# Kernel optimization log

Hardware: AMD Instinct MI355X
Metric: run time of the kernel (lower is better)

Reference implementation:

```python
import jax, jax.numpy as jnp
import numpy as np

B, N, IN_DIM, OUT = 4, 4096, 3, 40
NPTS = [1024, 256, 64, 16]   # base_points // sampling_ratio
K, FIRST_K = 8, 16
EPS = 1e-5

def gelu(t):
    return jax.nn.gelu(t, approximate=False)  # torch nn.GELU default (erf)

def pdist2(a, b):
    # a: (b,d,m), b: (b,d,n) -> squared pairwise distances (b,m,n)
    aa = jnp.sum(a * a, axis=1)[:, :, None]
    bb = jnp.sum(b * b, axis=1)[:, None, :]
    return aa + bb - 2.0 * jnp.einsum('bdm,bdn->bmn', a, b)

def knn_idx(a, b, k):
    # indices of k nearest points of b for each point of a
    return jax.lax.top_k(-pdist2(a, b), k)[1]

def gather_nbr(x, ind):
    # x: (b,d,n), ind: (b,m,k) -> (b,d,m,k)
    b, d, n = x.shape
    m, k = ind.shape[1], ind.shape[2]
    idx = jnp.broadcast_to(ind.reshape(b, 1, m * k), (b, d, m * k))
    return jnp.take_along_axis(x, idx, axis=2).reshape(b, d, m, k)

def bn(x):
    # BatchNorm (training-mode batch stats, gamma=1, beta=0 as at init)
    ax = (0,) + tuple(range(2, x.ndim))
    mu = jnp.mean(x, axis=ax, keepdims=True)
    var = jnp.mean((x - mu) ** 2, axis=ax, keepdims=True)
    return (x - mu) / jnp.sqrt(var + EPS)

def route(x, nbr):
    # (b,d,n),(b,n,k) -> (b,2d,n,k) : cat([neighbor - center, center])
    sel = gather_nbr(x, nbr)
    xc = x[:, :, :, None]
    return jnp.concatenate([sel - xc, jnp.broadcast_to(xc, sel.shape)], axis=1)

def edge_conv(x, l1, l2, sc, k, nbr=None):
    if nbr is None:
        nbr = knn_idx(x, x, k)  # dynamic graph in feature space
    h = jnp.max(jnp.einsum('of,bfnk->bonk', l1, route(x, nbr)), axis=-1)
    h = gelu(bn(h))
    h = jnp.max(jnp.einsum('of,bfnk->bonk', l2, route(h, nbr)), axis=-1)
    short = x if sc is None else jnp.einsum('of,bfn->bon', sc, x)
    return gelu(bn(short + h))

def fps(xyz, m):
    # farthest point sampling; xyz: (b,3,n) -> indices (b,m); start index 0
    pts = jnp.transpose(xyz, (0, 2, 1))  # (b,n,3)
    b, n, _ = pts.shape
    def body(carry, _):
        dmin, last = carry
        lp = jnp.take_along_axis(pts, last[:, None, None], axis=1)  # (b,1,3)
        d = jnp.sum((pts - lp) ** 2, axis=-1)
        dmin = jnp.minimum(dmin, d)
        nxt = jnp.argmax(dmin, axis=-1).astype(jnp.int32)
        return (dmin, nxt), last
    init = (jnp.full((b, n), jnp.inf, pts.dtype), jnp.zeros((b,), jnp.int32))
    _, inds = jax.lax.scan(body, init, None, length=m)
    return jnp.transpose(inds)  # (b,m)

def _forward(x, xyz, mlp_w, mlp_b, c0_l1, c0_l2, l1s, l2s, scs,
             head_w1, head_w2, head_b2):
    b = x.shape[0]
    nbr0 = knn_idx(xyz, xyz, FIRST_K)
    h = gelu(bn(jnp.einsum('oi,bin->bon', mlp_w, x) + mlp_b[None, :, None]))
    h = edge_conv(h, c0_l1, c0_l2, None, FIRST_K, nbr=nbr0)
    cur = xyz
    for i in range(4):
        m = NPTS[i]
        sind = fps(cur, m)
        sxyz = jnp.take_along_axis(
            cur, jnp.broadcast_to(sind[:, None, :], (b, cur.shape[1], m)), axis=2)
        nbr = knn_idx(sxyz, cur, K)
        cur = jnp.mean(gather_nbr(cur, nbr), axis=-1)      # sampled xyz = nbr mean
        h = jnp.max(gather_nbr(h, nbr), axis=-1)           # sampled feat = nbr max
        h = edge_conv(h, l1s[i], l2s[i], scs[i], K)
    g = jnp.mean(h, axis=-1)                               # global average pool
    g = gelu(bn(g @ head_w1.T))
    return g @ head_w2.T + head_b2[None, :]


def setup_inputs() -> dict:
    key = jax.random.key(0)
    ks = jax.random.split(key, 20)
    def w(k, o, i):
        return (jax.random.normal(k, (o, i), jnp.float32) / np.sqrt(i)).astype(jnp.float32)
    return {
        'x': jax.random.normal(ks[0], (B, IN_DIM, N), jnp.float32),
        'xyz': jax.random.normal(ks[1], (B, 3, N), jnp.float32),
        'mlp_w': w(ks[2], 64, IN_DIM), 'mlp_b': jnp.zeros((64,), jnp.float32),
        'c0_l1': w(ks[3], 64, 128), 'c0_l2': w(ks[4], 64, 128),
        's0_l1': w(ks[5], 64, 128), 's0_l2': w(ks[6], 64, 128),
        's1_l1': w(ks[7], 128, 128), 's1_l2': w(ks[8], 128, 256), 's1_sc': w(ks[9], 128, 64),
        's2_l1': w(ks[10], 256, 256), 's2_l2': w(ks[11], 256, 512), 's2_sc': w(ks[12], 256, 128),
        's3_l1': w(ks[13], 512, 512), 's3_l2': w(ks[14], 512, 1024), 's3_sc': w(ks[15], 512, 256),
        'head_w1': w(ks[16], 256, 512), 'head_w2': w(ks[17], OUT, 256),
        'head_b2': jnp.zeros((OUT,), jnp.float32),
    }


def reference(x, xyz, mlp_w, mlp_b, c0_l1, c0_l2, s0_l1, s0_l2,
              s1_l1, s1_l2, s1_sc, s2_l1, s2_l2, s2_sc, s3_l1, s3_l2, s3_sc,
              head_w1, head_w2, head_b2):
    return _forward(x, xyz, mlp_w, mlp_b, c0_l1, c0_l2,
                    (s0_l1, s1_l1, s2_l1, s3_l1),
                    (s0_l2, s1_l2, s2_l2, s3_l2),
                    (None, s1_sc, s2_sc, s3_sc),
                    head_w1, head_w2, head_b2)
```

## Files before the change

### kernel.cpp

```cpp
#include <hip/hip_runtime.h>
#include <math.h>

#define NCHUNK 32
typedef unsigned long long ull;

__device__ __forceinline__ float gelu_f(float v){
  return 0.5f*v*(1.0f+erff(v*0.70710678118654752440f));
}

__device__ __forceinline__ unsigned flipf(float d){
  unsigned u = __float_as_uint(d);
  return (u & 0x80000000u) ? ~u : (u | 0x80000000u);
}

template<int CTRL>
__device__ __forceinline__ ull dpp64(ull k){
  int lo = __builtin_amdgcn_update_dpp(0, (int)(unsigned)k,       CTRL, 0xF, 0xF, true);
  int hi = __builtin_amdgcn_update_dpp(0, (int)(unsigned)(k>>32), CTRL, 0xF, 0xF, true);
  return ((ull)(unsigned)hi<<32) | (unsigned)lo;
}
__device__ __forceinline__ ull rl64(ull k, int l){
  unsigned lo = (unsigned)__builtin_amdgcn_readlane((int)(unsigned)k, l);
  unsigned hi = (unsigned)__builtin_amdgcn_readlane((int)(unsigned)(k>>32), l);
  return ((ull)hi<<32) | lo;
}
__device__ __forceinline__ ull fmax64(ull a, ull b){
  return (ull)__double_as_longlong(fmax(__longlong_as_double((long long)a),
                                        __longlong_as_double((long long)b)));
}
__device__ __forceinline__ ull wave_fmax(ull k){
  k = fmax64(k, dpp64<0xB1>(k));
  k = fmax64(k, dpp64<0x4E>(k));
  k = fmax64(k, dpp64<0x141>(k));
  k = fmax64(k, dpp64<0x140>(k));
  ull a=rl64(k,0), b=rl64(k,16), c=rl64(k,32), d=rl64(k,48);
  return fmax64(fmax64(a,b), fmax64(c,d));
}
template<int CTRL>
__device__ __forceinline__ ull kmin_dpp(ull k){
  ull o = dpp64<CTRL>(k);
  return o < k ? o : k;
}
__device__ __forceinline__ ull wave_kmin(ull k){
  k = kmin_dpp<0xB1>(k);
  k = kmin_dpp<0x4E>(k);
  k = kmin_dpp<0x141>(k);
  k = kmin_dpp<0x140>(k);
  ull a=rl64(k,0), b=rl64(k,16), c=rl64(k,32), d=rl64(k,48);
  ull ab = a < b ? a : b, cd = c < d ? c : d;
  return ab < cd ? ab : cd;
}


template<int K, int T>
__device__ __forceinline__ void knn_body(
    const float* __restrict__ cand, int n,
    const float* __restrict__ qsrc, const int* __restrict__ qidx, int m,
    int* __restrict__ nbr, float* __restrict__ outc,
    int b, int qblk, char* smem)
{
  float* cx = (float*)smem; float* cy = cx+1024; float* cz = cy+1024; float* cbb = cz+1024;
  constexpr int NWV = T/64;
  int wv = threadIdx.x >> 6, lane = threadIdx.x & 63;
  int q = qblk*NWV + wv;
  const float* cb = cand + (size_t)b*3*n;
  int qi = qidx ? qidx[(size_t)b*m + q] : q;
  const float* qb = qsrc + (size_t)b*3*n;
  float qx = qb[qi], qy = qb[n+qi], qz = qb[2*n+qi];
  float aa = (qx*qx + qy*qy) + qz*qz;

  ull a[K];
  #pragma unroll
  for (int k=0;k<K;k++) a[k] = ~0ull;
  ull worst = ~0ull; int wslot = 0;

  for (int base=0; base<n; base+=1024){
    int cnt = min(1024, n-base);
    for (int j=threadIdx.x; j<cnt; j+=T){
      float x=cb[base+j], y=cb[n+base+j], z=cb[2*n+base+j];
      cx[j]=x; cy[j]=y; cz[j]=z; cbb[j]=(x*x+y*y)+z*z;
    }
    __syncthreads();
    int steps = cnt >> 6;
    for (int i=0;i<steps;i++){
      int j = lane + (i<<6);
      float d = aa + cbb[j] - 2.0f*((qx*cx[j]+qy*cy[j])+qz*cz[j]);
      ull key = ((ull)flipf(d)<<32) | (unsigned)(base+j);
      if (key < worst){
        #pragma unroll
        for (int k=0;k<K;k++) if (k==wslot) a[k] = key;
        worst = a[0]; wslot = 0;
        #pragma unroll
        for (int k=1;k<K;k++){
          bool g = a[k] > worst;
          worst = g ? a[k] : worst;
          wslot = g ? k : wslot;
        }
      }
    }
    __syncthreads();
  }

  #pragma unroll
  for (int kk=2; kk<=K; kk<<=1)
    #pragma unroll
    for (int jj=kk>>1; jj>0; jj>>=1)
      #pragma unroll
      for (int i=0;i<K;i++){
        int l = i ^ jj;
        if (l > i){
          bool dirUp = ((i & kk) == 0);
          ull x = a[i], y = a[l];
          bool sw = dirUp ? (x > y) : (x < y);
          a[i] = sw ? y : x;
          a[l] = sw ? x : y;
        }
      }

  ull head = a[0];
  int res[K];
  #pragma unroll
  for (int r=0; r<K; r++){
    ull mk = wave_kmin(head);
    res[r] = (int)(unsigned)mk;
    if (head == mk){
      #pragma unroll
      for (int i2=0;i2<K-1;i2++) a[i2]=a[i2+1];
      a[K-1] = ~0ull;
      head = a[0];
    }
  }
  if (lane == 0){
    int* o = nbr + ((size_t)b*m + q)*K;
    #pragma unroll
    for (int r=0;r<K;r++) o[r] = res[r];
  }
  if (outc != nullptr && lane < 3){
    const float* cd = cb + (size_t)lane*n;
    float s=0;
    #pragma unroll
    for (int k=0;k<K;k++) s += cd[res[k]];
    outc[((size_t)b*3 + lane)*m + q] = s * (1.0f/K);
  }
}

template<int NP, int T, int M>
__device__ __forceinline__ void fps_mw_seg(const float* __restrict__ cur, int n,
                                           int* __restrict__ sind, float* __restrict__ gdmin,
                                           int b, int M0, int M1, char* smem)
{
  constexpr int NW = T/64;
  int tid = threadIdx.x;
  int wv = tid>>6;
  const float* cb = cur + (size_t)b*3*n;
  float4* lp = (float4*)smem;
  ull* wred = (ull*)(smem + sizeof(float4)*NP*T);
  float* gd = gdmin + (size_t)b*n;
  float px[NP], py[NP], pz[NP], dmin[NP];
  unsigned nj[NP];
  #pragma unroll
  for (int s=0;s<NP;s++){
    int j = tid + s*T;
    px[s]=cb[j]; py[s]=cb[n+j]; pz[s]=cb[2*n+j];
    dmin[s] = (M0==0) ? 1e30f : gd[j];
    nj[s] = (unsigned)(~j);
    lp[j] = make_float4(px[s],py[s],pz[s],0.f);
  }
  __syncthreads();
  int ci = (M0==0) ? 0 : sind[(size_t)b*M + (M0-1)];
  float4 w0 = lp[ci];
  float X = w0.x, Y = w0.y, Z = w0.z;
  if (M0==0 && tid==0) sind[(size_t)b*M] = 0;
  __builtin_amdgcn_s_setprio(3);
  int p = 0;
  int s0 = (M0==0) ? 1 : M0;
  for (int step=s0; step<M1; step++){
    ull key[NP];
    #pragma unroll
    for (int s=0;s<NP;s++){
      float dx=px[s]-X, dy=py[s]-Y, dz=pz[s]-Z;
      float d = (dx*dx + dy*dy) + dz*dz;
      float nd = fminf(dmin[s], d);
      dmin[s] = nd;
      key[s] = ((ull)__float_as_uint(nd)<<32) | nj[s];
    }
    #pragma unroll
    for (int w=NP; w>1; w>>=1)
      #pragma unroll
      for (int i=0;i<NP;i++) if (i < (w>>1))
        key[i] = fmax64(key[i], key[i+(w>>1)]);
    ull wk = wave_fmax(key[0]);
    if ((tid&63)==0) wred[p*NW + wv] = wk;
    __syncthreads();
    ull gk = wred[p*NW];
    #pragma unroll
    for (int w=1;w<NW;w++) gk = fmax64(gk, wred[p*NW + w]);
    int gi = (int)(~(unsigned)gk);
    if (tid==0) sind[(size_t)b*M + step] = gi;
    float4 wp = lp[gi];
    X=wp.x; Y=wp.y; Z=wp.z;
    p ^= 1;
  }
  __builtin_amdgcn_s_setprio(0);
  #pragma unroll
  for (int s=0;s<NP;s++) gd[tid + s*T] = dmin[s];
}

template<int NP, int M>
__device__ __forceinline__ void fps_sw_body(const float* __restrict__ cur, int n,
                                            int* __restrict__ sind, int b, char* smem)
{
  int lane = threadIdx.x;
  const float* cb = cur + (size_t)b*3*n;
  float4* lp = (float4*)smem;
  float px[NP], py[NP], pz[NP], dmin[NP];
  unsigned nj[NP];
  #pragma unroll
  for (int s=0;s<NP;s++){
    int j = lane + s*64;
    px[s]=cb[j]; py[s]=cb[n+j]; pz[s]=cb[2*n+j]; dmin[s]=1e30f;
    nj[s] = (unsigned)(~j);
    lp[j] = make_float4(px[s],py[s],pz[s],0.f);
  }
  float X = lp[0].x, Y = lp[0].y, Z = lp[0].z;
  if (lane==0) sind[(size_t)b*M] = 0;
  __builtin_amdgcn_s_setprio(3);
  for (int step=1; step<M; step++){
    ull key[NP];
    #pragma unroll
    for (int s=0;s<NP;s++){
      float dx=px[s]-X, dy=py[s]-Y, dz=pz[s]-Z;
      float d = (dx*dx + dy*dy) + dz*dz;
      float nd = fminf(dmin[s], d);
      dmin[s] = nd;
      key[s] = ((ull)__float_as_uint(nd)<<32) | nj[s];
    }
    #pragma unroll
    for (int w=NP; w>1; w>>=1)
      #pragma unroll
      for (int i=0;i<NP;i++) if (i < (w>>1))
        key[i] = fmax64(key[i], key[i+(w>>1)]);
    ull gk = wave_fmax(key[0]);
    int gi = (int)(~(unsigned)gk);
    if (lane==0) sind[(size_t)b*M + step] = gi;
    float4 wp = lp[gi];
    X=wp.x; Y=wp.y; Z=wp.z;
  }
  __builtin_amdgcn_s_setprio(0);
}

template<bool DUAL, bool BN>
__device__ __forceinline__ void gemm_body(
    const float* __restrict__ A, const float* __restrict__ B,
    float* __restrict__ out0, float* __restrict__ out1,
    int M, int N, int Kd, int lda, int ldb, int ldo, int boff,
    long sA, long sB, long sO, const float* __restrict__ part, float invR,
    int bxi, int byi, int bzi, char* smem)
{
  A += (size_t)bzi * sA; B += (size_t)bzi * sB;
  float* o0 = out0 + (size_t)bzi * sO;
  float* o1 = DUAL ? (out1 + (size_t)bzi * sO) : nullptr;
  int rowBase = byi*64, colBase = bxi*64;
  float (*As)[64]  = (float(*)[64])smem;
  float (*Bs0)[64] = (float(*)[64])(smem + 4096);
  float (*Bs1)[64] = (float(*)[64])(smem + 8192);
  float* mu_s = (float*)(smem + 12288);
  float* var_s = mu_s + 512;
  int tid = threadIdx.x;
  if (BN){
    for (int oo=tid; oo<Kd; oo+=blockDim.x){
      float s=0, q=0;
      #pragma unroll 4
      for (int c=0;c<NCHUNK;c++){
        s += part[(size_t)c*1024 + oo];
        q += part[(size_t)(NCHUNK+c)*1024 + oo];
      }
      float mu = s*invR;
      mu_s[oo] = mu;
      var_s[oo] = q*invR - mu*mu;
    }
    __syncthreads();
  }
  int ty = tid>>4, tx = tid&15;
  float acc0[4][4] = {}, acc1[4][4] = {};
  int lr = tid>>2, lk = (tid&3)*4;
  for (int k0=0; k0<Kd; k0+=16) {
    float4 va = make_float4(0,0,0,0);
    int r = rowBase + lr;
    if (r < M) va = *(const float4*)(A + (size_t)r*lda + k0 + lk);
    if (BN){
      int c = k0 + lk;
      va.x = gelu_f((va.x - mu_s[c+0]) / sqrtf(var_s[c+0] + 1e-5f));
      va.y = gelu_f((va.y - mu_s[c+1]) / sqrtf(var_s[c+1] + 1e-5f));
      va.z = gelu_f((va.z - mu_s[c+2]) / sqrtf(var_s[c+2] + 1e-5f));
      va.w = gelu_f((va.w - mu_s[c+3]) / sqrtf(var_s[c+3] + 1e-5f));
    }
    As[lk+0][lr]=va.x; As[lk+1][lr]=va.y; As[lk+2][lr]=va.z; As[lk+3][lr]=va.w;
    float4 vb = make_float4(0,0,0,0), vb2 = make_float4(0,0,0,0);
    int c2 = colBase + lr;
    if (c2 < N) {
      vb = *(const float4*)(B + (size_t)c2*ldb + k0 + lk);
      if (DUAL) vb2 = *(const float4*)(B + (size_t)c2*ldb + boff + k0 + lk);
    }
    Bs0[lk+0][lr]=vb.x; Bs0[lk+1][lr]=vb.y; Bs0[lk+2][lr]=vb.z; Bs0[lk+3][lr]=vb.w;
    if (DUAL) {
      Bs1[lk+0][lr]=vb2.x-vb.x; Bs1[lk+1][lr]=vb2.y-vb.y;
      Bs1[lk+2][lr]=vb2.z-vb.z; Bs1[lk+3][lr]=vb2.w-vb.w;
    }
    __syncthreads();
    #pragma unroll
    for (int kk=0;kk<16;kk++){
      float4 a  = *(const float4*)&As[kk][ty*4];
      float4 b0 = *(const float4*)&Bs0[kk][tx*4];
      float av[4]={a.x,a.y,a.z,a.w};
      float b0v[4]={b0.x,b0.y,b0.z,b0.w};
      #pragma unroll
      for (int i=0;i<4;i++)
        #pragma unroll
        for (int j=0;j<4;j++) acc0[i][j] = fmaf(av[i], b0v[j], acc0[i][j]);
      if (DUAL) {
        float4 b1 = *(const float4*)&Bs1[kk][tx*4];
        float b1v[4]={b1.x,b1.y,b1.z,b1.w};
        #pragma unroll
        for (int i=0;i<4;i++)
          #pragma unroll
          for (int j=0;j<4;j++) acc1[i][j] = fmaf(av[i], b1v[j], acc1[i][j]);
      }
    }
    __syncthreads();
  }
  #pragma unroll
  for (int i=0;i<4;i++){
    int r = rowBase + ty*4 + i;
    if (r < M) {
      #pragma unroll
      for (int j=0;j<4;j++){
        int c = colBase + tx*4 + j;
        if (c < N) {
          o0[(size_t)r*ldo + c] = acc0[i][j];
          if (DUAL) o1[(size_t)r*ldo + c] = acc1[i][j];
        }
      }
    }
  }
}

template<bool DUAL, bool BN>
__device__ __forceinline__ void gemm_body_g(
    const float* __restrict__ A, const float* __restrict__ B,
    float* __restrict__ out0, float* __restrict__ out1,
    int M, int N, int Kd, int lda, int ldb, int ldo, int boff,
    const float* __restrict__ part, float invR,
    int bxi, int byi, char* smem)
{
  int rowBase = byi*64, colBase = bxi*64;
  float (*As)[64]  = (float(*)[64])smem;
  float (*Bs0)[64] = (float(*)[64])(smem + 4096);
  float (*Bs1)[64] = (float(*)[64])(smem + 8192);
  float* mu_s = (float*)(smem + 12288);
  float* var_s = mu_s + 512;
  int tid = threadIdx.x;
  bool act = tid < 256;
  if (BN){
    for (int oo=tid; oo<Kd; oo+=blockDim.x){
      float s=0, q=0;
      #pragma unroll 4
      for (int c=0;c<NCHUNK;c++){
        s += part[(size_t)c*1024 + oo];
        q += part[(size_t)(NCHUNK+c)*1024 + oo];
      }
      float mu = s*invR;
      mu_s[oo] = mu;
      var_s[oo] = q*invR - mu*mu;
    }
    __syncthreads();
  }
  int ty = tid>>4, tx = tid&15;
  float acc0[4][4] = {}, acc1[4][4] = {};
  int lr = tid>>2, lk = (tid&3)*4;
  for (int k0=0; k0<Kd; k0+=16) {
    if (act){
      float4 va = make_float4(0,0,0,0);
      int r = rowBase + lr;
      if (r < M) va = *(const float4*)(A + (size_t)r*lda + k0 + lk);
      if (BN){
        int c = k0 + lk;
        va.x = gelu_f((va.x - mu_s[c+0]) / sqrtf(var_s[c+0] + 1e-5f));
        va.y = gelu_f((va.y - mu_s[c+1]) / sqrtf(var_s[c+1] + 1e-5f));
        va.z = gelu_f((va.z - mu_s[c+2]) / sqrtf(var_s[c+2] + 1e-5f));
        va.w = gelu_f((va.w - mu_s[c+3]) / sqrtf(var_s[c+3] + 1e-5f));
      }
      As[lk+0][lr]=va.x; As[lk+1][lr]=va.y; As[lk+2][lr]=va.z; As[lk+3][lr]=va.w;
      float4 vb = make_float4(0,0,0,0), vb2 = make_float4(0,0,0,0);
      int c2 = colBase + lr;
      if (c2 < N) {
        vb = *(const float4*)(B + (size_t)c2*ldb + k0 + lk);
        if (DUAL) vb2 = *(const float4*)(B + (size_t)c2*ldb + boff + k0 + lk);
      }
      Bs0[lk+0][lr]=vb.x; Bs0[lk+1][lr]=vb.y; Bs0[lk+2][lr]=vb.z; Bs0[lk+3][lr]=vb.w;
      if (DUAL) {
        Bs1[lk+0][lr]=vb2.x-vb.x; Bs1[lk+1][lr]=vb2.y-vb.y;
        Bs1[lk+2][lr]=vb2.z-vb.z; Bs1[lk+3][lr]=vb2.w-vb.w;
      }
    }
    __syncthreads();
    if (act){
      #pragma unroll
      for (int kk=0;kk<16;kk++){
        float4 a  = *(const float4*)&As[kk][ty*4];
        float4 b0 = *(const float4*)&Bs0[kk][tx*4];
        float av[4]={a.x,a.y,a.z,a.w};
        float b0v[4]={b0.x,b0.y,b0.z,b0.w};
        #pragma unroll
        for (int i=0;i<4;i++)
          #pragma unroll
          for (int j=0;j<4;j++) acc0[i][j] = fmaf(av[i], b0v[j], acc0[i][j]);
        if (DUAL) {
          float4 b1 = *(const float4*)&Bs1[kk][tx*4];
          float b1v[4]={b1.x,b1.y,b1.z,b1.w};
          #pragma unroll
          for (int i=0;i<4;i++)
            #pragma unroll
            for (int j=0;j<4;j++) acc1[i][j] = fmaf(av[i], b1v[j], acc1[i][j]);
        }
      }
    }
    __syncthreads();
  }
  if (act){
    #pragma unroll
    for (int i=0;i<4;i++){
      int r = rowBase + ty*4 + i;
      if (r < M) {
        #pragma unroll
        for (int j=0;j<4;j++){
          int c = colBase + tx*4 + j;
          if (c < N) {
            out0[(size_t)r*ldo + c] = acc0[i][j];
            if (DUAL) out1[(size_t)r*ldo + c] = acc1[i][j];
          }
        }
      }
    }
  }
}

__device__ __forceinline__ void gather_elem(
    const float* __restrict__ P, const int* __restrict__ nbr,
    const float* __restrict__ addA, const float* __restrict__ addB,
    float* __restrict__ out, int n_out, int n_src, int O, int K, int total, int e)
{
  if (e >= total) return;
  int o = e % O; int r = e / O;
  int b = r / n_out; int i = r % n_out;
  const int* nb = nbr + ((size_t)b*n_out + i)*K;
  float mx = -1e38f;
  for (int k=0;k<K;k++){
    int j = nb[k];
    float v = P[((size_t)b*n_src + j)*O + o];
    mx = fmaxf(mx, v);
  }
  float res = mx;
  if (addA) res += addA[e];
  if (addB) res = addB[e] + res;
  out[e] = res;
}

__device__ __forceinline__ void gatherbn_body(
    const float* __restrict__ P, const int* __restrict__ nbr,
    const float* __restrict__ part, float invR,
    float* __restrict__ out, float* __restrict__ aa,
    int n_out, int n_src, int O, int K, int blk, char* smem)
{
  float* mu_s = (float*)smem; float* var_s = mu_s + 256; float* sv = var_s + 256;
  int tid = threadIdx.x;
  for (int oo=tid; oo<O; oo+=256){
    float s=0, q=0;
    #pragma unroll 4
    for (int c=0;c<NCHUNK;c++){
      s += part[(size_t)c*1024 + oo];
      q += part[(size_t)(NCHUNK+c)*1024 + oo];
    }
    float mu = s*invR;
    mu_s[oo] = mu;
    var_s[oo] = q*invR - mu*mu;
  }
  __syncthreads();
  int e = blk*256 + tid;
  int o = e % O; int r = e / O;
  int b = r / n_out; int i = r % n_out;
  const int* nb = nbr + ((size_t)b*n_out + i)*K;
  float mu = mu_s[o], sd = sqrtf(var_s[o] + 1e-5f);
  float mx = -1e38f;
  for (int k=0;k<K;k++){
    int j = nb[k];
    float p = P[((size_t)b*n_src + j)*O + o];
    float v = gelu_f((p - mu)/sd);
    mx = fmaxf(mx, v);
  }
  out[e] = mx;
  sv[tid] = mx*mx;
  __syncthreads();
  for (int st=O>>1; st>0; st>>=1){
    if (o < st) sv[tid] += sv[tid+st];
    __syncthreads();
  }
  if (o == 0) aa[r] = sv[tid];
}


#define FPS_SMEM 65664

__global__ __launch_bounds__(512,2) void mega1(
    const float* __restrict__ xyz, const float* __restrict__ x,
    const float* __restrict__ mlpw, const float* __restrict__ mlpb,
    int* __restrict__ sind0, float* __restrict__ gdmin,
    int* __restrict__ nbr0, float* __restrict__ hA, int M0, int M1)
{
  __shared__ __align__(16) char SMEM[FPS_SMEM];
  int bid = blockIdx.x;
  if (bid < 4){
    fps_mw_seg<8,512,1024>(xyz, 4096, sind0, gdmin, bid, M0, M1, SMEM);
  } else if (bid < 4+2048){
    int kb = bid - 4;
    knn_body<16,512>(xyz, 4096, xyz, nullptr, 4096, nbr0, nullptr, kb>>9, kb&511, SMEM);
  } else {
    int e = (bid - 2052)*512 + threadIdx.x;
    if (e < 4*4096*64){
      int o = e & 63; int r = e >> 6;
      int b = r / 4096; int i = r % 4096;
      const float* xb = x + (size_t)b*3*4096;
      hA[e] = ((mlpw[o*3+0]*xb[i] + mlpw[o*3+1]*xb[4096+i]) + mlpw[o*3+2]*xb[2*4096+i]) + mlpb[o];
    }
  }
}

__global__ __launch_bounds__(512,2) void fps_bngelu(
    const float* fcur, int* sind, float* gdmin, int M0, int M1,
    float* __restrict__ xx, const float* __restrict__ part, float invR, int O, int total)
{
  __shared__ __align__(16) char SMEM[FPS_SMEM];
  if (blockIdx.x < 4){
    fps_mw_seg<8,512,1024>(fcur, 4096, sind, gdmin, blockIdx.x, M0, M1, SMEM);
    return;
  }
  float* mu_s = (float*)SMEM; float* var_s = mu_s + 512;
  for (int oo=threadIdx.x; oo<O; oo+=512){
    float s=0, q=0;
    #pragma unroll 4
    for (int c=0;c<NCHUNK;c++){
      s += part[(size_t)c*1024 + oo];
      q += part[(size_t)(NCHUNK+c)*1024 + oo];
    }
    float mu = s*invR;
    mu_s[oo] = mu;
    var_s[oo] = q*invR - mu*mu;
  }
  __syncthreads();
  int e = (blockIdx.x-4)*512 + threadIdx.x;
  if (e >= total) return;
  int o = e % O;
  float v = (xx[e]-mu_s[o]) / sqrtf(var_s[o] + 1e-5f);
  xx[e] = gelu_f(v);
}

template<bool DUAL, bool BN>
__global__ __launch_bounds__(512,2) void fps0_gemm(
    const float* fcur, int* sind, float* gdmin, int M0, int M1,
    const float* A, const float* B, float* out0, float* out1,
    int Mg, int Ng, int Kd, int lda, int ldb, int ldo, int boff,
    const float* part, float invR, int nbx)
{
  __shared__ __align__(16) char SMEM[FPS_SMEM];
  if (blockIdx.x < 4){
    fps_mw_seg<8,512,1024>(fcur, 4096, sind, gdmin, blockIdx.x, M0, M1, SMEM);
    return;
  }
  int l = blockIdx.x - 4;
  gemm_body_g<DUAL,BN>(A,B,out0,out1,Mg,Ng,Kd,lda,ldb,ldo,boff,part,invR, l%nbx, l/nbx, SMEM);
}

__global__ __launch_bounds__(512,2) void fps0_gather(
    const float* fcur, int* sind, float* gdmin, int M0, int M1,
    const float* P, const int* nbr, const float* addA, const float* addB,
    float* out, int n_out, int n_src, int O, int K, int total)
{
  __shared__ __align__(16) char SMEM[FPS_SMEM];
  if (blockIdx.x < 4){
    fps_mw_seg<8,512,1024>(fcur, 4096, sind, gdmin, blockIdx.x, M0, M1, SMEM);
    return;
  }
  int e = (blockIdx.x-4)*512 + threadIdx.x;
  gather_elem(P, nbr, addA, addB, out, n_out, n_src, O, K, total, e);
}

__global__ __launch_bounds__(512,2) void fps0_stats(
    const float* fcur, int* sind, float* gdmin, int M0, int M1,
    const float* __restrict__ x, int R, int O, float* __restrict__ part)
{
  __shared__ __align__(16) char SMEM[FPS_SMEM];
  if (blockIdx.x < 4){
    fps_mw_seg<8,512,1024>(fcur, 4096, sind, gdmin, blockIdx.x, M0, M1, SMEM);
    return;
  }
  int o = threadIdx.x;
  if (o >= O) return;
  int chunk = blockIdx.x - 4;
  int per = (R + NCHUNK - 1)/NCHUNK;
  int r0 = chunk*per, r1 = min(r0+per, R);
  float s=0, q=0;
  for (int r=r0; r<r1; r++){ float v = x[(size_t)r*O + o]; s+=v; q+=v*v; }
  part[(size_t)chunk*1024 + o] = s;
  part[(size_t)(NCHUNK+chunk)*1024 + o] = q;
}

__global__ __launch_bounds__(256) void knn_wave8(
    const float* cand, int n, const float* qsrc, const int* qidx, int m,
    int* nbr, float* outc)
{
  __shared__ __align__(16) char SMEM[16384];
  knn_body<8,256>(cand, n, qsrc, qidx, m, nbr, outc, blockIdx.y, blockIdx.x, SMEM);
}

template<int NP, int M>
__global__ __launch_bounds__(256) void fps_gatherbn(
    const float* fcur, int fn, int* sind,
    const float* P, const int* nbr, const float* part, float invR,
    float* out, float* aa, int n_out, int n_src, int O, int K)
{
  __shared__ __align__(16) char SMEM[(NP*64*16 > 16384) ? NP*64*16 : 16384];
  if (blockIdx.x < 4){
    if (threadIdx.x < 64) fps_sw_body<NP,M>(fcur, fn, sind, blockIdx.x, SMEM);
    return;
  }
  gatherbn_body(P, nbr, part, invR, out, aa, n_out, n_src, O, K, blockIdx.x-4, SMEM);
}

template<int NP, int M, bool DUAL, bool BN>
__global__ __launch_bounds__(256) void fps_gemm(
    const float* fcur, int fn, int* sind,
    const float* A, const float* B, float* out0, float* out1,
    int Mg, int Ng, int Kd, int lda, int ldb, int ldo, int boff,
    const float* part, float invR, int nbx, int nby)
{
  __shared__ __align__(16) char SMEM[(NP*64*16 > 16896) ? NP*64*16 : 16896];
  if (blockIdx.x < 4){
    if (threadIdx.x < 64) fps_sw_body<NP,M>(fcur, fn, sind, blockIdx.x, SMEM);
    return;
  }
  int l = blockIdx.x - 4;
  int bx = l % nbx, by = (l/nbx) % nby, bz = l/(nbx*nby);
  gemm_body<DUAL,BN>(A,B,out0,out1,Mg,Ng,Kd,lda,ldb,ldo,boff,0,0,0,part,invR,bx,by,bz,SMEM);
}

__global__ __launch_bounds__(256) void knn_gather(
    const float* cand, int n, const float* qsrc, const int* qidx, int m,
    int* nbrOut, float* outc, int KNB,
    const float* P, const int* nbr, const float* addA, const float* addB,
    float* out, int n_out, int n_src, int O, int K, int total)
{
  __shared__ __align__(16) char SMEM[16384];
  if (blockIdx.x < KNB){
    int qpb = m/4;
    knn_body<8,256>(cand, n, qsrc, qidx, m, nbrOut, outc, blockIdx.x/qpb, blockIdx.x%qpb, SMEM);
    return;
  }
  gather_elem(P, nbr, addA, addB, out, n_out, n_src, O, K, total, (blockIdx.x-KNB)*256 + threadIdx.x);
}

__global__ __launch_bounds__(256) void knn_gemm(
    const float* cand, int n, const float* qsrc, const int* qidx, int m,
    int* nbrOut, float* outc, int KNB,
    const float* A, const float* B, float* out0,
    int Mg, int Ng, int Kd, int lda, int ldb, int ldo,
    long sA, long sB, long sO, int nbx, int nby)
{
  __shared__ __align__(16) char SMEM[16896];
  if (blockIdx.x < KNB){
    int qpb = m/4;
    knn_body<8,256>(cand, n, qsrc, qidx, m, nbrOut, outc, blockIdx.x/qpb, blockIdx.x%qpb, SMEM);
    return;
  }
  int l = blockIdx.x - KNB;
  int bx = l % nbx, by = (l/nbx) % nby, bz = l/(nbx*nby);
  gemm_body<false,false>(A,B,out0,nullptr,Mg,Ng,Kd,lda,ldb,ldo,0,sA,sB,sO,nullptr,0.f,bx,by,bz,SMEM);
}

template<bool DUAL, bool BN>
__global__ __launch_bounds__(256) void gemm_nt(
    const float* A, const float* B, float* out0, float* out1,
    int M, int N, int Kd, int lda, int ldb, int ldo, int boff,
    long sA, long sB, long sO, const float* part, float invR)
{
  __shared__ __align__(16) char SMEM[16896];
  gemm_body<DUAL,BN>(A,B,out0,out1,M,N,Kd,lda,ldb,ldo,boff,sA,sB,sO,part,invR,
                     blockIdx.x, blockIdx.y, blockIdx.z, SMEM);
}

__global__ __launch_bounds__(256) void gemm2sc(
    const float* A2, const float* B2, float* o20, float* o21, int R, int O2, int O1v,
    const float* part, float invR,
    const float* Asc, const float* Bsc, float* osc, int Cin,
    int nbx, int nby)
{
  __shared__ __align__(16) char SMEM[16896];
  int l = blockIdx.x;
  int half = nbx*nby;
  if (l < half){
    gemm_body<true,true>(A2,B2,o20,o21,R,O2,O1v,O1v,2*O1v,O2,O1v,0,0,0,part,invR, l%nbx, l/nbx, 0, SMEM);
  } else {
    l -= half;
    gemm_body<false,false>(Asc,Bsc,osc,nullptr,R,O2,Cin,Cin,Cin,O2,0,0,0,0,nullptr,0.f, l%nbx, l/nbx, 0, SMEM);
  }
}

__global__ __launch_bounds__(256) void gathermax_kernel(
    const float* P, const int* nbr, const float* addA, const float* addB,
    float* out, int n_out, int n_src, int O, int K, int total)
{
  gather_elem(P, nbr, addA, addB, out, n_out, n_src, O, K, total, blockIdx.x*256 + threadIdx.x);
}

__global__ __launch_bounds__(256) void gatherbn_kernel(
    const float* P, const int* nbr, const float* part, float invR,
    float* out, float* aa, int n_out, int n_src, int O, int K)
{
  __shared__ __align__(16) char SMEM[3072];
  gatherbn_body(P, nbr, part, invR, out, aa, n_out, n_src, O, K, blockIdx.x, SMEM);
}

template<int K>
__global__ __launch_bounds__(256) void topk_wave(
    const float* __restrict__ G, const float* __restrict__ aa, int m,
    int* __restrict__ nbr)
{
  __shared__ float abs_s[1024];
  int b = blockIdx.y;
  int wv = threadIdx.x >> 6, lane = threadIdx.x & 63;
  int q = blockIdx.x*4 + wv;
  const float* ab = aa + (size_t)b*m;
  for (int j=threadIdx.x; j<m; j+=256) abs_s[j] = ab[j];
  __syncthreads();
  float aq = ab[q];
  const float* Gq = G + ((size_t)b*m + q)*m;

  ull a[K];
  #pragma unroll
  for (int k=0;k<K;k++) a[k] = ~0ull;
  ull worst = ~0ull; int wslot = 0;

  int steps = (m+63)>>6;
  for (int i=0;i<steps;i++){
    int j = lane + (i<<6);
    ull key = ~0ull;
    if (j < m){
      float g = Gq[j];
      float d = aq + abs_s[j] - 2.0f*g;
      key = ((ull)flipf(d)<<32) | (unsigned)j;
    }
    if (key < worst){
      #pragma unroll
      for (int k=0;k<K;k++) if (k==wslot) a[k] = key;
      worst = a[0]; wslot = 0;
      #pragma unroll
      for (int k=1;k<K;k++){
        bool g = a[k] > worst;
        worst = g ? a[k] : worst;
        wslot = g ? k : wslot;
      }
    }
  }
  #pragma unroll
  for (int kk=2; kk<=K; kk<<=1)
    #pragma unroll
    for (int jj=kk>>1; jj>0; jj>>=1)
      #pragma unroll
      for (int i=0;i<K;i++){
        int l = i ^ jj;
        if (l > i){
          bool dirUp = ((i & kk) == 0);
          ull x = a[i], y = a[l];
          bool sw = dirUp ? (x > y) : (x < y);
          a[i] = sw ? y : x;
          a[l] = sw ? x : y;
        }
      }
  ull head = a[0];
  int res[K];
  #pragma unroll
  for (int r=0; r<K; r++){
    ull mk = wave_kmin(head);
    res[r] = (int)(unsigned)mk;
    if (head == mk){
      #pragma unroll
      for (int i2=0;i2<K-1;i2++) a[i2]=a[i2+1];
      a[K-1] = ~0ull;
      head = a[0];
    }
  }
  if (lane == 0){
    int* o = nbr + ((size_t)b*m + q)*K;
    #pragma unroll
    for (int r=0;r<K;r++) o[r] = res[r];
  }
}

__global__ void stats_part_kernel(const float* __restrict__ x, int R, int O,
                                  float* __restrict__ part)
{
  int o = threadIdx.x;
  int chunk = blockIdx.x;
  int per = (R + NCHUNK - 1)/NCHUNK;
  int r0 = chunk*per, r1 = min(r0+per, R);
  float s=0, q=0;
  for (int r=r0; r<r1; r++){ float v = x[(size_t)r*O + o]; s+=v; q+=v*v; }
  part[(size_t)chunk*1024 + o] = s;
  part[(size_t)(NCHUNK+chunk)*1024 + o] = q;
}

__global__ __launch_bounds__(1024) void head_kernel(const float* __restrict__ h,
    const float* __restrict__ part, float invR,
    const float* __restrict__ w1, const float* __restrict__ w2,
    const float* __restrict__ b2, float* __restrict__ out)
{
  __shared__ __align__(16) float mu_s[512], var_s[512];
  __shared__ __align__(16) float g[4*512];
  __shared__ __align__(16) float t[4*256];
  int tid = threadIdx.x;
  for (int oo=tid; oo<512; oo+=1024){
    float s=0, q=0;
    #pragma unroll 4
    for (int c=0;c<NCHUNK;c++){
      s += part[(size_t)c*1024 + oo];
      q += part[(size_t)(NCHUNK+c)*1024 + oo];
    }
    float mu = s*invR;
    mu_s[oo] = mu;
    var_s[oo] = q*invR - mu*mu;
  }
  __syncthreads();
  for (int e=tid; e<2048; e+=1024){
    int b=e>>9, c=e&511;
    float mu = mu_s[c], sd = sqrtf(var_s[c] + 1e-5f);
    float s=0;
    for (int p=0;p<16;p++){
      float v = h[((size_t)(b*16+p))*512 + c];
      s += gelu_f((v-mu)/sd);
    }
    g[e] = s * (1.0f/16.0f);
  }
  __syncthreads();
  {
    int b = tid>>8, j = tid&255;
    const float4* gr = (const float4*)(g + b*512);
    const float4* wr = (const float4*)(w1 + (size_t)j*512);
    float s=0;
    for (int c=0;c<128;c++){
      float4 a=gr[c], w=wr[c];
      s = fmaf(a.x,w.x, fmaf(a.y,w.y, fmaf(a.z,w.z, fmaf(a.w,w.w, s))));
    }
    t[tid] = s;
  }
  __syncthreads();
  if (tid < 256){
    float v0=t[tid], v1=t[256+tid], v2=t[512+tid], v3=t[768+tid];
    float mu = ((v0+v1)+v2+v3)*0.25f;
    float d0=v0-mu, d1=v1-mu, d2=v2-mu, d3=v3-mu;
    float var = ((d0*d0+d1*d1)+d2*d2+d3*d3)*0.25f;
    float sq = sqrtf(var + 1e-5f);
    t[tid]     = gelu_f(d0/sq);
    t[256+tid] = gelu_f(d1/sq);
    t[512+tid] = gelu_f(d2/sq);
    t[768+tid] = gelu_f(d3/sq);
  }
  __syncthreads();
  if (tid < 160){
    int b = tid/40, o = tid%40;
    const float* tr = t + b*256; const float* wr = w2 + (size_t)o*256;
    float s=0;
    for (int j=0;j<256;j++) s = fmaf(tr[j], wr[j], s);
    out[tid] = s + b2[o];
  }
}

extern "C" void kernel_launch(void* const* d_in, const int* in_sizes, int n_in,
                              void* d_out, int out_size, void* d_ws, size_t ws_size,
                              hipStream_t stream)
{
  const float* x    = (const float*)d_in[0];
  const float* xyz  = (const float*)d_in[1];
  const float* mlpw = (const float*)d_in[2];
  const float* mlpb = (const float*)d_in[3];
  const float* c0l1 = (const float*)d_in[4];
  const float* c0l2 = (const float*)d_in[5];
  const float* L1[4] = {(const float*)d_in[6], (const float*)d_in[8],
                        (const float*)d_in[11], (const float*)d_in[14]};
  const float* L2[4] = {(const float*)d_in[7], (const float*)d_in[9],
                        (const float*)d_in[12], (const float*)d_in[15]};
  const float* SC[4] = {nullptr, (const float*)d_in[10],
                        (const float*)d_in[13], (const float*)d_in[16]};
  const float* hw1 = (const float*)d_in[17];
  const float* hw2 = (const float*)d_in[18];
  const float* hb2 = (const float*)d_in[19];
  float* out = (float*)d_out;

  float* ws = (float*)d_ws;
  const size_t MF = 1024*1024;
  float* D    = ws;
  float* hA   = ws + 4*MF;
  float* hX   = ws + 5*MF;
  float* hP   = ws + 6*MF;
  float* hCT  = ws + 7*MF;
  float* hSH  = ws + 8*MF;
  float* hH1  = ws + 9*MF;
  float* hOUT = ws + 10*MF;
  float* aux  = ws + 11*MF;
  int*   nbr0  = (int*)aux;                 aux += 262144;
  int*   nbrS0 = (int*)aux;                 aux += 32768;
  int*   nbrS1 = (int*)aux;                 aux += 8192;
  int*   nbrS2 = (int*)aux;                 aux += 2048;
  int*   nbrS3 = (int*)aux;                 aux += 512;
  int*   nbrF  = (int*)aux;                 aux += 32768;
  int*   sind0 = (int*)aux;                 aux += 4096;
  int*   sind1 = (int*)aux;                 aux += 1024;
  int*   sind2 = (int*)aux;                 aux += 256;
  int*   sind3 = (int*)aux;                 aux += 64;
  float* aa    = aux;                       aux += 4096;
  float* cur1  = aux;                       aux += 12288;
  float* cur2  = aux;                       aux += 3072;
  float* cur3  = aux;                       aux += 768;
  float* part  = aux;                       aux += 65536;
  float* gdmin = aux;                       aux += 16384;

  int tot0 = 4*4096*64;

  mega1<<<4100, 512, 0, stream>>>(xyz, x, mlpw, mlpb, sind0, gdmin, nbr0, hA, 0, 260);
  stats_part_kernel<<<NCHUNK, 64, 0, stream>>>(hA, 16384, 64, part);
  fps_bngelu<<<4+2048, 512, 0, stream>>>(xyz, sind0, gdmin, 260, 387, hA, part, 1.0f/16384.0f, 64, tot0);
  fps0_gemm<true,false><<<4+256, 512, 0, stream>>>(xyz, sind0, gdmin, 387, 514,
      hA, c0l1, hP, hCT, 16384, 64, 64, 64, 128, 64, 64, nullptr, 0.f, 1);
  fps0_gather<<<4+2048, 512, 0, stream>>>(xyz, sind0, gdmin, 514, 641,
      hP, nbr0, hCT, nullptr, hH1, 4096, 4096, 64, 16, 1048576);
  stats_part_kernel<<<NCHUNK, 64, 0, stream>>>(hH1, 16384, 64, part);
  fps0_gemm<true,true><<<4+256, 512, 0, stream>>>(xyz, sind0, gdmin, 641, 768,
      hH1, c0l2, hP, hCT, 16384, 64, 64, 64, 128, 64, 64, part, 1.0f/16384.0f, 1);
  fps0_gather<<<4+2048, 512, 0, stream>>>(xyz, sind0, gdmin, 768, 895,
      hP, nbr0, hCT, hA, hOUT, 4096, 4096, 64, 16, 1048576);
  fps0_stats<<<4+NCHUNK, 512, 0, stream>>>(xyz, sind0, gdmin, 895, 1024,
      hOUT, 16384, 64, part);

  knn_wave8<<<dim3(256,4),256,0,stream>>>(xyz, 4096, xyz, sind0, 1024, nbrS0, cur1);

  fps_gatherbn<16,256><<<4+1024,256,0,stream>>>(cur1, 1024, sind1,
      hOUT, nbrS0, part, 1.0f/16384.0f, hX, aa, 1024, 4096, 64, 8);
  knn_gemm<<<256+1024,256,0,stream>>>(cur1, 1024, cur1, sind1, 256, nbrS1, cur2, 256,
      hX, hX, D, 1024, 1024, 64, 64, 64, 1024,
      (long)1024*64, (long)1024*64, (long)1024*1024, 16, 16);
  topk_wave<8><<<dim3(256,4),256,0,stream>>>(D, aa, 1024, nbrF);
  fps_gemm<4,64,true,false><<<4+64,256,0,stream>>>(cur2, 256, sind2,
      hX, L1[0], hP, hCT, 4096, 64, 64, 64, 128, 64, 64, nullptr, 0.f, 1, 64);
  knn_gather<<<64+1024,256,0,stream>>>(cur2, 256, cur2, sind2, 64, nbrS2, cur3, 64,
      hP, nbrF, hCT, nullptr, hH1, 1024, 1024, 64, 8, 262144);
  stats_part_kernel<<<NCHUNK, 64, 0, stream>>>(hH1, 4096, 64, part);
  fps_gemm<1,16,true,true><<<4+64,256,0,stream>>>(cur3, 64, sind3,
      hH1, L2[0], hP, hCT, 4096, 64, 64, 64, 128, 64, 64, part, 1.0f/4096.0f, 1, 64);
  knn_gather<<<16+1024,256,0,stream>>>(cur3, 64, cur3, sind3, 16, nbrS3, nullptr, 16,
      hP, nbrF, hCT, hX, hA, 1024, 1024, 64, 8, 262144);
  stats_part_kernel<<<NCHUNK, 64, 0, stream>>>(hA, 4096, 64, part);

  const int   mArr[3]   = {256, 64, 16};
  const int   nsrcArr[3]= {1024, 256, 64};
  const int   CinArr[3] = {64, 128, 256};
  const int   OArr[3]   = {128, 256, 512};
  const int*  nbrSs[3]  = {nbrS1, nbrS2, nbrS3};
  float* hcur = hA;
  float invRprev = 1.0f/4096.0f;
  for (int s=0;s<3;s++){
    int m = mArr[s], nsrc = nsrcArr[s], Cin = CinArr[s], O1 = OArr[s], O2 = OArr[s];
    int R = 4*m;
    int th = R*Cin;
    gatherbn_kernel<<<th/256,256,0,stream>>>(hcur, nbrSs[s], part, invRprev,
                                             hX, aa, m, nsrc, Cin, 8);
    dim3 gp((m+63)/64, (m+63)/64, 4);
    gemm_nt<false,false><<<gp,256,0,stream>>>(hX, hX, D, nullptr, m, m, Cin, Cin, Cin, m, 0,
                                              (long)m*Cin, (long)m*Cin, (long)m*m, nullptr, 0.f);
    topk_wave<8><<<dim3(m/4,4),256,0,stream>>>(D, aa, m, nbrF);
    dim3 gg1((O1+63)/64, (R+63)/64, 1);
    gemm_nt<true,false><<<gg1,256,0,stream>>>(hX, L1[s+1], hP, hCT, R, O1, Cin, Cin, 2*Cin, O1, Cin, 0,0,0, nullptr, 0.f);
    int t1 = R*O1;
    gathermax_kernel<<<(t1+255)/256,256,0,stream>>>(hP, nbrF, hCT, nullptr, hH1, m, m, O1, 8, t1);
    stats_part_kernel<<<NCHUNK, O1, 0, stream>>>(hH1, R, O1, part);
    int nbx = (O2+63)/64, nby = (R+63)/64;
    gemm2sc<<<2*nbx*nby,256,0,stream>>>(hH1, L2[s+1], hP, hCT, R, O2, O1, part, 1.0f/R,
                                        hX, SC[s+1], hSH, Cin, nbx, nby);
    int t2 = R*O2;
    float* outbuf = (s&1) ? hA : hOUT;
    gathermax_kernel<<<(t2+255)/256,256,0,stream>>>(hP, nbrF, hCT, hSH, outbuf, m, m, O2, 8, t2);
    stats_part_kernel<<<NCHUNK, O2, 0, stream>>>(outbuf, R, O2, part);
    hcur = outbuf;
    invRprev = 1.0f/R;
  }

  head_kernel<<<1,1024,0,stream>>>(hcur, part, 1.0f/64.0f, hw1, hw2, hb2, out);
}
```

Baseline: 1.774 ms.

## Overlap first half of sampled-point kNN with FPS segment kernel

```diff
diff --git a/kernel.cpp b/kernel.cpp
--- a/kernel.cpp
+++ b/kernel.cpp
@@ -57,12 +57,12 @@
     const float* __restrict__ cand, int n,
     const float* __restrict__ qsrc, const int* __restrict__ qidx, int m,
     int* __restrict__ nbr, float* __restrict__ outc,
-    int b, int qblk, char* smem)
-{
-  float* cx = (float*)smem; float* cy = cx+1024; float* cz = cy+1024; float* cbb = cz+1024;
+    int b, int qblk, int qoff, char* smem)
+{
+  float4* tile = (float4*)smem;
   constexpr int NWV = T/64;
   int wv = threadIdx.x >> 6, lane = threadIdx.x & 63;
-  int q = qblk*NWV + wv;
+  int q = qblk*NWV + wv + qoff;
   const float* cb = cand + (size_t)b*3*n;
   int qi = qidx ? qidx[(size_t)b*m + q] : q;
   const float* qb = qsrc + (size_t)b*3*n;
@@ -78,13 +78,14 @@
     int cnt = min(1024, n-base);
     for (int j=threadIdx.x; j<cnt; j+=T){
       float x=cb[base+j], y=cb[n+base+j], z=cb[2*n+base+j];
-      cx[j]=x; cy[j]=y; cz[j]=z; cbb[j]=(x*x+y*y)+z*z;
+      tile[j] = make_float4(x,y,z,(x*x+y*y)+z*z);
     }
     __syncthreads();
     int steps = cnt >> 6;
     for (int i=0;i<steps;i++){
       int j = lane + (i<<6);
-      float d = aa + cbb[j] - 2.0f*((qx*cx[j]+qy*cy[j])+qz*cz[j]);
+      float4 c = tile[j];
+      float d = aa + c.w - 2.0f*((qx*c.x+qy*c.y)+qz*c.z);
       ull key = ((ull)flipf(d)<<32) | (unsigned)(base+j);
       if (key < worst){
         #pragma unroll
@@ -192,9 +193,10 @@
     ull wk = wave_fmax(key[0]);
     if ((tid&63)==0) wred[p*NW + wv] = wk;
     __syncthreads();
-    ull gk = wred[p*NW];
-    #pragma unroll
-    for (int w=1;w<NW;w++) gk = fmax64(gk, wred[p*NW + w]);
+    const ulonglong2* wp2 = (const ulonglong2*)(wred + p*NW);
+    ulonglong2 m0 = wp2[0], m1 = wp2[1], m2 = wp2[2], m3 = wp2[3];
+    ull gk = fmax64(fmax64(fmax64(m0.x,m0.y), fmax64(m1.x,m1.y)),
+                    fmax64(fmax64(m2.x,m2.y), fmax64(m3.x,m3.y)));
     int gi = (int)(~(unsigned)gk);
     if (tid==0) sind[(size_t)b*M + step] = gi;
     float4 wp = lp[gi];
@@ -523,7 +525,7 @@
     fps_mw_seg<8,512,1024>(xyz, 4096, sind0, gdmin, bid, M0, M1, SMEM);
   } else if (bid < 4+2048){
     int kb = bid - 4;
-    knn_body<16,512>(xyz, 4096, xyz, nullptr, 4096, nbr0, nullptr, kb>>9, kb&511, SMEM);
+    knn_body<16,512>(xyz, 4096, xyz, nullptr, 4096, nbr0, nullptr, kb>>9, kb&511, 0, SMEM);
   } else {
     int e = (bid - 2052)*512 + threadIdx.x;
     if (e < 4*4096*64){
@@ -578,6 +580,27 @@
   }
   int l = blockIdx.x - 4;
   gemm_body_g<DUAL,BN>(A,B,out0,out1,Mg,Ng,Kd,lda,ldb,ldo,boff,part,invR, l%nbx, l/nbx, SMEM);
+}
+
+__global__ __launch_bounds__(512,2) void fps0_gather_knn(
+    const float* fcur, int* sind, float* gdmin, int M0, int M1,
+    const float* cand, int n, const float* qsrc, const int* qidx, int m,
+    int* nbrOut, float* outc, int KNB,
+    const float* P, const int* nbr, const float* addA, const float* addB,
+    float* out, int n_out, int n_src, int O, int K, int total)
+{
+  __shared__ __align__(16) char SMEM[FPS_SMEM];
+  if (blockIdx.x < 4){
+    fps_mw_seg<8,512,1024>(fcur, 4096, sind, gdmin, blockIdx.x, M0, M1, SMEM);
+    return;
+  }
+  int l = blockIdx.x - 4;
+  if (l < KNB){
+    knn_body<8,512>(cand, n, qsrc, qidx, m, nbrOut, outc, l>>6, l&63, 0, SMEM);
+    return;
+  }
+  int e = (l-KNB)*512 + threadIdx.x;
+  gather_elem(P, nbr, addA, addB, out, n_out, n_src, O, K, total, e);
 }
 
 __global__ __launch_bounds__(512,2) void fps0_gather(
@@ -615,11 +638,11 @@
 }
 
 __global__ __launch_bounds__(256) void knn_wave8(
-    const float* cand, int n, const float* qsrc, const int* qidx, int m,
+    const float* cand, int n, const float* qsrc, const int* qidx, int m, int qoff,
     int* nbr, float* outc)
 {
   __shared__ __align__(16) char SMEM[16384];
-  knn_body<8,256>(cand, n, qsrc, qidx, m, nbr, outc, blockIdx.y, blockIdx.x, SMEM);
+  knn_body<8,256>(cand, n, qsrc, qidx, m, nbr, outc, blockIdx.y, blockIdx.x, qoff, SMEM);
 }
 
 template<int NP, int M>
@@ -662,7 +685,7 @@
   __shared__ __align__(16) char SMEM[16384];
   if (blockIdx.x < KNB){
     int qpb = m/4;
-    knn_body<8,256>(cand, n, qsrc, qidx, m, nbrOut, outc, blockIdx.x/qpb, blockIdx.x%qpb, SMEM);
+    knn_body<8,256>(cand, n, qsrc, qidx, m, nbrOut, outc, blockIdx.x/qpb, blockIdx.x%qpb, 0, SMEM);
     return;
   }
   gather_elem(P, nbr, addA, addB, out, n_out, n_src, O, K, total, (blockIdx.x-KNB)*256 + threadIdx.x);
@@ -678,7 +701,7 @@
   __shared__ __align__(16) char SMEM[16896];
   if (blockIdx.x < KNB){
     int qpb = m/4;
-    knn_body<8,256>(cand, n, qsrc, qidx, m, nbrOut, outc, blockIdx.x/qpb, blockIdx.x%qpb, SMEM);
+    knn_body<8,256>(cand, n, qsrc, qidx, m, nbrOut, outc, blockIdx.x/qpb, blockIdx.x%qpb, 0, SMEM);
     return;
   }
   int l = blockIdx.x - KNB;
@@ -936,20 +959,21 @@
 
   mega1<<<4100, 512, 0, stream>>>(xyz, x, mlpw, mlpb, sind0, gdmin, nbr0, hA, 0, 260);
   stats_part_kernel<<<NCHUNK, 64, 0, stream>>>(hA, 16384, 64, part);
-  fps_bngelu<<<4+2048, 512, 0, stream>>>(xyz, sind0, gdmin, 260, 387, hA, part, 1.0f/16384.0f, 64, tot0);
-  fps0_gemm<true,false><<<4+256, 512, 0, stream>>>(xyz, sind0, gdmin, 387, 514,
+  fps_bngelu<<<4+2048, 512, 0, stream>>>(xyz, sind0, gdmin, 260, 390, hA, part, 1.0f/16384.0f, 64, tot0);
+  fps0_gemm<true,false><<<4+256, 512, 0, stream>>>(xyz, sind0, gdmin, 390, 517,
       hA, c0l1, hP, hCT, 16384, 64, 64, 64, 128, 64, 64, nullptr, 0.f, 1);
-  fps0_gather<<<4+2048, 512, 0, stream>>>(xyz, sind0, gdmin, 514, 641,
+  fps0_gather_knn<<<4+256+2048, 512, 0, stream>>>(xyz, sind0, gdmin, 517, 644,
+      xyz, 4096, xyz, sind0, 1024, nbrS0, cur1, 256,
       hP, nbr0, hCT, nullptr, hH1, 4096, 4096, 64, 16, 1048576);
   stats_part_kernel<<<NCHUNK, 64, 0, stream>>>(hH1, 16384, 64, part);
-  fps0_gemm<true,true><<<4+256, 512, 0, stream>>>(xyz, sind0, gdmin, 641, 768,
+  fps0_gemm<true,true><<<4+256, 512, 0, stream>>>(xyz, sind0, gdmin, 644, 771,
       hH1, c0l2, hP, hCT, 16384, 64, 64, 64, 128, 64, 64, part, 1.0f/16384.0f, 1);
-  fps0_gather<<<4+2048, 512, 0, stream>>>(xyz, sind0, gdmin, 768, 895,
+  fps0_gather<<<4+2048, 512, 0, stream>>>(xyz, sind0, gdmin, 771, 898,
       hP, nbr0, hCT, hA, hOUT, 4096, 4096, 64, 16, 1048576);
-  fps0_stats<<<4+NCHUNK, 512, 0, stream>>>(xyz, sind0, gdmin, 895, 1024,
+  fps0_stats<<<4+NCHUNK, 512, 0, stream>>>(xyz, sind0, gdmin, 898, 1024,
       hOUT, 16384, 64, part);
 
-  knn_wave8<<<dim3(256,4),256,0,stream>>>(xyz, 4096, xyz, sind0, 1024, nbrS0, cur1);
+  knn_wave8<<<dim3(128,4),256,0,stream>>>(xyz, 4096, xyz, sind0, 1024, 512, nbrS0, cur1);
 
   fps_gatherbn<16,256><<<4+1024,256,0,stream>>>(cur1, 1024, sind1,
       hOUT, nbrS0, part, 1.0f/16384.0f, hX, aa, 1024, 4096, 64, 8);
```

After: 1.755 ms. No clear change (-1.1%).
